# Kernel tuning notes

Hardware: AMD Instinct MI355X
Metric: run time of the kernel (lower is better)

## Reference

```python
import jax, jax.numpy as jnp
import numpy as np

N, B, E, H, D, L, NT = 30000, 16, 60000, 128, 64, 2, 5


def _build_graph():
    rng = np.random.default_rng(0)
    ng = N // B
    row = rng.integers(0, N, size=E)
    g = row // ng
    col = g * ng + rng.integers(0, ng, size=E)  # bonds stay within a graph
    order = np.argsort(g, kind='stable')        # sort bonds by graph id
    row, col = row[order], col[order]
    edge_index = np.stack([row, col]).astype(np.int32)
    # bond graph: bonds adjacent iff they share an atom (vectorized _build_bond_graph)
    atoms = np.concatenate([row, col])
    bonds = np.concatenate([np.arange(E), np.arange(E)])
    o2 = np.argsort(atoms, kind='stable')
    sb = bonds[o2]
    counts = np.bincount(atoms, minlength=N)
    offs = np.concatenate([[0], np.cumsum(counts)[:-1]])
    sq = counts * counts
    total = int(sq.sum())
    gid = np.repeat(np.arange(N), sq)
    poff = np.concatenate([[0], np.cumsum(sq)[:-1]])
    pos = np.arange(total) - np.repeat(poff, sq)
    c, o = counts[gid], offs[gid]
    ii, jj = pos // c, pos % c
    mask = ii != jj
    bond_edge_index = np.stack([sb[o + ii][mask], sb[o + jj][mask]]).astype(np.int32)
    batch = np.repeat(np.arange(B), ng).astype(np.int32)
    return edge_index, bond_edge_index, batch


def setup_inputs() -> dict:
    edge_index, bond_edge_index, batch = _build_graph()
    key = jax.random.key(0)
    ks = jax.random.split(key, 16)
    s = 0.05
    n = lambda k, shp: jax.random.normal(k, shp, jnp.float32) * s
    return {
        'atom_features': jax.random.normal(ks[0], (N, H), jnp.float32),
        'atom_pos': jax.random.normal(ks[1], (N, 3), jnp.float32),
        'atomic_numbers': jax.random.randint(ks[2], (N,), 1, 20, jnp.int32),
        'batch': jnp.asarray(batch),
        'edge_index': jnp.asarray(edge_index),
        'bond_edge_index': jnp.asarray(bond_edge_index),
        'iw1': n(ks[3], (2 * H, D)), 'ib1': jnp.zeros((D,), jnp.float32),
        'iw2': n(ks[4], (D, D)), 'ib2': jnp.zeros((D,), jnp.float32),
        'emb': n(ks[5], (L, NT, D)),
        'mw1': n(ks[6], (L, 3 * D, D)), 'mb1': jnp.zeros((L, D), jnp.float32),
        'mw2': n(ks[7], (L, D, D)), 'mb2': jnp.zeros((L, D), jnp.float32),
        'uw1': n(ks[8], (L, 2 * D, D)), 'ub1': jnp.zeros((L, D), jnp.float32),
        'uw2': n(ks[9], (L, D, D)), 'ub2': jnp.zeros((L, D), jnp.float32),
        'num_graphs': B,
    }


def reference(atom_features, atom_pos, iw1, ib1, iw2, ib2, emb, mw1, mb1, mw2, mb2,
              uw1, ub1, uw2, ub2, atomic_numbers, batch, edge_index, bond_edge_index,
              num_graphs):
    row, col = edge_index
    hi, hj = atom_features[row], atom_features[col]  # [E, H] gathers
    # bond_init MLP
    x = jax.nn.silu(jnp.concatenate([hi, hj], -1) @ iw1 + ib1) @ iw2 + ib2  # [E, D]
    # _classify_bonds: cosine-similarity thresholds (order matters, matches torch)
    ni = jnp.maximum(jnp.linalg.norm(hi, axis=-1), 1e-8)
    nj = jnp.maximum(jnp.linalg.norm(hj, axis=-1), 1e-8)
    sim = jnp.sum(hi * hj, -1) / (ni * nj)
    bt = jnp.where(sim > 0.8, 1, 0)
    bt = jnp.where(sim > 0.9, 2, bt)
    bt = jnp.where(sim < 0.3, 3, bt)
    src, dst = bond_edge_index  # x_j = x[src], x_i = x[dst]; aggregate at dst
    nb = x.shape[0]
    deg = jax.ops.segment_sum(jnp.ones(src.shape, jnp.float32), dst, num_segments=nb)
    denom = jnp.maximum(deg, 1.0)[:, None]  # PyG mean aggr: 0 for isolated nodes
    for l in range(mw1.shape[0]):
        te = emb[l][bt]  # [E, D] bond-type embedding
        msg_in = jnp.concatenate([x[dst], x[src], te[dst]], -1)  # [BE, 3D]
        msg = jax.nn.silu(msg_in @ mw1[l] + mb1[l]) @ mw2[l] + mb2[l]
        aggr = jax.ops.segment_sum(msg, dst, num_segments=nb) / denom
        upd_in = jnp.concatenate([aggr, x], -1)
        x = x + jax.nn.silu(upd_in @ uw1[l] + ub1[l]) @ uw2[l] + ub2[l]
    # pooling: edges are sorted by graph, so repeat_interleave == batch[row]
    bond_batch = batch[row]
    cnt = jax.ops.segment_sum(jnp.ones((nb,), jnp.float32), bond_batch, num_segments=num_graphs)
    gfeat = jax.ops.segment_sum(x, bond_batch, num_segments=num_graphs) / jnp.maximum(cnt, 1.0)[:, None]
    return x, gfeat
```

## Files before the change

kernel.cpp:

```cpp
#include <hip/hip_runtime.h>
#include <hip/hip_cooperative_groups.h>
#include <cstdint>
#include <cstddef>

namespace cg = cooperative_groups;

#define HDIM 128
#define DDIM 64
#define NTYPES 5
#define NGRAPHS 16
#define EPB 64
#define SCAP 1024
#define PREPB 132

typedef __attribute__((ext_vector_type(8))) short short8;
typedef __attribute__((ext_vector_type(4))) float f32x4;

static __device__ __forceinline__ short8 as_s8(uint4 u) {
    return __builtin_bit_cast(short8, u);
}

static __device__ __forceinline__ float silu_f(float v) {
    return v * __builtin_amdgcn_rcpf(1.0f + __expf(-v));
}

static __device__ __forceinline__ float4 ld4(const float* p) {
    return *reinterpret_cast<const float4*>(p);
}

static __device__ __forceinline__ void st4(float* p, float4 v) {
    *reinterpret_cast<float4*>(p) = v;
}

static __device__ __forceinline__ float4 add4(float4 a, float4 b) {
    return make_float4(a.x + b.x, a.y + b.y, a.z + b.z, a.w + b.w);
}

static __device__ __forceinline__ void silu_acc4(float4& s, float4 v) {
    s.x += silu_f(v.x);
    s.y += silu_f(v.y);
    s.z += silu_f(v.z);
    s.w += silu_f(v.w);
}

static __device__ __forceinline__ unsigned int bf16r(float f) {
    unsigned int u = __float_as_uint(f);
    return (u + 0x7FFFu + ((u >> 16) & 1u)) >> 16;
}
static __device__ __forceinline__ unsigned int cvtpk(float a, float b) {
    unsigned int r;
    asm("v_cvt_pk_bf16_f32 %0, %1, %2" : "=v"(r) : "v"(a), "v"(b));
    return r;
}
static __device__ __forceinline__ uint4 pack8(const float* f) {
    uint4 r;
    r.x = cvtpk(f[0], f[1]);
    r.y = cvtpk(f[2], f[3]);
    r.z = cvtpk(f[4], f[5]);
    r.w = cvtpk(f[6], f[7]);
    return r;
}
static __device__ __forceinline__ void unpack8(uint4 u, float4& a, float4& b) {
    a.x = __uint_as_float(u.x << 16);
    a.y = __uint_as_float(u.x & 0xFFFF0000u);
    a.z = __uint_as_float(u.y << 16);
    a.w = __uint_as_float(u.y & 0xFFFF0000u);
    b.x = __uint_as_float(u.z << 16);
    b.y = __uint_as_float(u.z & 0xFFFF0000u);
    b.z = __uint_as_float(u.w << 16);
    b.w = __uint_as_float(u.w & 0xFFFF0000u);
}

static __device__ __forceinline__ void hilo8(const float* f, uint4& h, uint4& lo) {
    h = pack8(f);
    float4 a, b;
    unpack8(h, a, b);
    lo.x = cvtpk(f[0] - a.x, f[1] - a.y);
    lo.y = cvtpk(f[2] - a.z, f[3] - a.w);
    lo.z = cvtpk(f[4] - b.x, f[5] - b.y);
    lo.w = cvtpk(f[6] - b.z, f[7] - b.w);
}

static __device__ __forceinline__ int xcd_logical_block() {
    int chunk = (int)(gridDim.x >> 3);
    return (int)(blockIdx.x & 7) * chunk + (int)(blockIdx.x >> 3);
}

__global__ void __launch_bounds__(256) bsum_k(const int* __restrict__ cnt,
                                              int* __restrict__ bsum, int E) {
    __shared__ int red[256];
    int t = threadIdx.x;
    int i = blockIdx.x * 256 + t;
    red[t] = (i < E) ? cnt[i] : 0;
    __syncthreads();
    #pragma unroll
    for (int off = 128; off > 0; off >>= 1) {
        if (t < off) red[t] += red[t + off];
        __syncthreads();
    }
    if (t == 0) bsum[blockIdx.x] = red[0];
}

__global__ void __launch_bounds__(1024) bscan_k(const int* __restrict__ bsum,
                                                int* __restrict__ bpre, int NB) {
    __shared__ int sh[1024];
    int t = threadIdx.x;
    int v0 = (t < NB) ? bsum[t] : 0;
    sh[t] = v0;
    __syncthreads();
    for (int off = 1; off < 1024; off <<= 1) {
        int v = (t >= off) ? sh[t - off] : 0;
        __syncthreads();
        sh[t] += v;
        __syncthreads();
    }
    if (t < NB) bpre[t] = sh[t] - v0;
}

__global__ void __launch_bounds__(256) offs_k(const int* __restrict__ cnt,
                                              const int* __restrict__ bpre,
                                              int* __restrict__ offs,
                                              int* __restrict__ cursor, int E) {
    __shared__ int sh[256];
    int t = threadIdx.x;
    int i = blockIdx.x * 256 + t;
    int v0 = (i < E) ? cnt[i] : 0;
    sh[t] = v0;
    __syncthreads();
    for (int off = 1; off < 256; off <<= 1) {
        int v = (t >= off) ? sh[t - off] : 0;
        __syncthreads();
        sh[t] += v;
        __syncthreads();
    }
    int ex = sh[t] - v0 + bpre[blockIdx.x];
    if (i < E) { offs[i] = ex; cursor[i] = ex; }
    if (i == E - 1) offs[E] = ex + v0;
}

__global__ void __launch_bounds__(256) scatter_k(const int* __restrict__ bsrc,
                                                 const int* __restrict__ bdst,
                                                 int* __restrict__ cursor,
                                                 int* __restrict__ srclist, int BE) {
    int i = blockIdx.x * 256 + threadIdx.x;
    if (i < BE) {
        int d = bdst[i];
        int p = __hip_atomic_fetch_add(&cursor[d], 1, __ATOMIC_RELAXED,
                                       __HIP_MEMORY_SCOPE_AGENT);
        srclist[p] = bsrc[i];
    }
}

static __device__ void dev_prep(int b, int l,
                                const float* __restrict__ emb,
                                const float* __restrict__ mw1,
                                const float* __restrict__ mb1,
                                const float* __restrict__ mw2,
                                const float* __restrict__ mb2,
                                const float* __restrict__ uw1,
                                const float* __restrict__ uw2,
                                const float* __restrict__ iw2,
                                const float* __restrict__ iw1,
                                float* __restrict__ tt,
                                float* __restrict__ b2u,
                                uint4* __restrict__ fw2u,
                                uint4* __restrict__ fu1b,
                                uint4* __restrict__ fu2,
                                uint4* __restrict__ fp,
                                uint4* __restrict__ fiw2,
                                uint4* __restrict__ fp0,
                                uint4* __restrict__ fiw1) {
    if (b < 10) {
        int ll = b / NTYPES, t = b % NTYPES;
        const float* embl = emb + (size_t)ll * NTYPES * DDIM + (size_t)t * DDIM;
        const float* w1 = mw1 + (size_t)ll * 192 * DDIM;
        float s = mb1[ll * DDIM + l];
        #pragma unroll 8
        for (int k = 0; k < DDIM; ++k)
            s = fmaf(embl[k], w1[(HDIM + k) * DDIM + l], s);
        tt[(size_t)b * DDIM + l] = s;
        return;
    }
    if (b < 12) {
        int ll = b - 10;
        const float* u1 = uw1 + (size_t)ll * 128 * DDIM;
        float s = 0.f;
        #pragma unroll 8
        for (int t = 0; t < DDIM; ++t)
            s = fmaf(mb2[ll * DDIM + t], u1[(size_t)t * DDIM + l], s);
        b2u[ll * DDIM + l] = s;
        return;
    }
    int pb = b - 12;
    int mat = pb >> 3, jt = (pb >> 1) & 3, ks = pb & 1;
    int k0 = ks * 32 + (l >> 4) * 8;
    int j = jt * 16 + (l & 15);
    float f[8];
    uint4* dst;
    if (mat <= 1) {
        const float* w2 = mw2 + (size_t)mat * DDIM * DDIM;
        const float* u1 = uw1 + (size_t)mat * 128 * DDIM;
        #pragma unroll
        for (int i = 0; i < 8; ++i) {
            float s = 0.f;
            #pragma unroll 8
            for (int t = 0; t < DDIM; ++t)
                s = fmaf(w2[(size_t)(k0 + i) * DDIM + t], u1[(size_t)t * DDIM + j], s);
            f[i] = s;
        }
        dst = fw2u + (size_t)mat * 1024;
    } else {
        const float* src;
        switch (mat) {
            case 2:  src = uw1 + 64 * 64;                    dst = fu1b;        break;
            case 3:  src = uw1 + 128 * 64 + 64 * 64;         dst = fu1b + 1024; break;
            case 4:  src = uw2;                              dst = fu2;         break;
            case 5:  src = uw2 + 4096;                       dst = fu2 + 1024;  break;
            case 6:  src = mw1 + (size_t)192 * 64;           dst = fp;          break;
            case 7:  src = mw1 + (size_t)192 * 64 + 64 * 64; dst = fp + 1024;   break;
            case 8:  src = iw2;                              dst = fiw2;        break;
            case 9:  src = mw1;                              dst = fp0;         break;
            case 10: src = mw1 + (size_t)64 * 64;            dst = fp0 + 1024;  break;
            case 11: src = iw1;                              dst = fiw1;        break;
            case 12: src = iw1 + (size_t)64 * 64;            dst = fiw1 + 1024; break;
            case 13: src = iw1 + (size_t)128 * 64;           dst = fiw1 + 2048; break;
            default: src = iw1 + (size_t)192 * 64;           dst = fiw1 + 3072; break;
        }
        #pragma unroll
        for (int i = 0; i < 8; ++i) f[i] = src[(size_t)(k0 + i) * DDIM + j];
    }
    uint4 h, lo;
    hilo8(f, h, lo);
    size_t di = ((size_t)(jt * 2 + ks) * 64 + l) * 2;
    dst[di] = h;
    dst[di + 1] = lo;
}

__global__ void __launch_bounds__(256) prepcount_k(
    const float* __restrict__ emb, const float* __restrict__ mw1,
    const float* __restrict__ mb1, const float* __restrict__ mw2,
    const float* __restrict__ mb2, const float* __restrict__ uw1,
    const float* __restrict__ uw2, const float* __restrict__ iw2,
    const float* __restrict__ iw1,
    float* __restrict__ tt, float* __restrict__ b2u,
    uint4* __restrict__ fw2u, uint4* __restrict__ fu1b, uint4* __restrict__ fu2,
    uint4* __restrict__ fp, uint4* __restrict__ fiw2, uint4* __restrict__ fp0,
    uint4* __restrict__ fiw1,
    const int* __restrict__ bdst, int* __restrict__ cnt, int BE) {
    int b = blockIdx.x;
    if (b < PREPB) {
        if (threadIdx.x < 64)
            dev_prep(b, threadIdx.x, emb, mw1, mb1, mw2, mb2, uw1, uw2, iw2, iw1,
                     tt, b2u, fw2u, fu1b, fu2, fp, fiw2, fp0, fiw1);
        return;
    }
    int i = (b - PREPB) * 256 + threadIdx.x;
    if (i < BE)
        __hip_atomic_fetch_add(&cnt[bdst[i]], 1, __ATOMIC_RELAXED, __HIP_MEMORY_SCOPE_AGENT);
}

static __device__ __forceinline__ int slotIdx(int row, int slot) {
    return row * 8 + (slot ^ (row & 7));
}
static __device__ __forceinline__ int slotIdx16(int row, int slot) {
    return row * 16 + (slot ^ (row & 7));
}

static __device__ __forceinline__ short8 ldFragA(const uint4* buf, int rowBase, int lane, int ks) {
    int row = rowBase + (lane & 15);
    int slot = ks * 4 + (lane >> 4);
    return as_s8(buf[slotIdx(row, slot)]);
}
static __device__ __forceinline__ short8 ldFragA16(const uint4* buf, int rowBase, int lane, int slot0) {
    int row = rowBase + (lane & 15);
    int slot = slot0 + (lane >> 4);
    return as_s8(buf[slotIdx16(row, slot)]);
}

static __device__ __forceinline__ void loadB(const uint4* __restrict__ frag, int jt, int lane,
                                             short8& h0, short8& h1, short8& l0, short8& l1) {
    const uint4* p0 = frag + ((size_t)(jt * 2 + 0) * 64 + lane) * 2;
    const uint4* p1 = frag + ((size_t)(jt * 2 + 1) * 64 + lane) * 2;
    h0 = as_s8(p0[0]); l0 = as_s8(p0[1]);
    h1 = as_s8(p1[0]); l1 = as_s8(p1[1]);
}

static __device__ __forceinline__ f32x4 gemm_tile(const uint4* Ahi, const uint4* Alo,
        int rowBase, int lane,
        short8 bh0, short8 bh1, short8 bl0, short8 bl1, f32x4 acc) {
    short8 ah0 = ldFragA(Ahi, rowBase, lane, 0);
    short8 ah1 = ldFragA(Ahi, rowBase, lane, 1);
    short8 al0 = ldFragA(Alo, rowBase, lane, 0);
    short8 al1 = ldFragA(Alo, rowBase, lane, 1);
    acc = __builtin_amdgcn_mfma_f32_16x16x32_bf16(ah0, bh0, acc, 0, 0, 0);
    acc = __builtin_amdgcn_mfma_f32_16x16x32_bf16(ah1, bh1, acc, 0, 0, 0);
    acc = __builtin_amdgcn_mfma_f32_16x16x32_bf16(al0, bh0, acc, 0, 0, 0);
    acc = __builtin_amdgcn_mfma_f32_16x16x32_bf16(al1, bh1, acc, 0, 0, 0);
    acc = __builtin_amdgcn_mfma_f32_16x16x32_bf16(ah0, bl0, acc, 0, 0, 0);
    acc = __builtin_amdgcn_mfma_f32_16x16x32_bf16(ah1, bl1, acc, 0, 0, 0);
    return acc;
}

static __device__ __forceinline__ f32x4 gemm_tile16(const uint4* Ahi, const uint4* Alo,
        int rowBase, int lane, int sb,
        short8 bh0, short8 bh1, short8 bl0, short8 bl1, f32x4 acc) {
    short8 ah0 = ldFragA16(Ahi, rowBase, lane, sb + 0);
    short8 ah1 = ldFragA16(Ahi, rowBase, lane, sb + 4);
    short8 al0 = ldFragA16(Alo, rowBase, lane, sb + 0);
    short8 al1 = ldFragA16(Alo, rowBase, lane, sb + 4);
    acc = __builtin_amdgcn_mfma_f32_16x16x32_bf16(ah0, bh0, acc, 0, 0, 0);
    acc = __builtin_amdgcn_mfma_f32_16x16x32_bf16(ah1, bh1, acc, 0, 0, 0);
    acc = __builtin_amdgcn_mfma_f32_16x16x32_bf16(al0, bh0, acc, 0, 0, 0);
    acc = __builtin_amdgcn_mfma_f32_16x16x32_bf16(al1, bh1, acc, 0, 0, 0);
    acc = __builtin_amdgcn_mfma_f32_16x16x32_bf16(ah0, bl0, acc, 0, 0, 0);
    acc = __builtin_amdgcn_mfma_f32_16x16x32_bf16(ah1, bl1, acc, 0, 0, 0);
    return acc;
}

static __device__ __forceinline__ void dev_atom_proj(
    int a0, int tid, int lane, int w,
    const float* __restrict__ AF, const uint4* __restrict__ fIw1,
    float* __restrict__ pa, float* __restrict__ qa, float* __restrict__ na, int N,
    uint4* sHi, uint4* sLo) {
    {
        int dl = tid >> 3, q = tid & 7;
        int a = a0 + dl;
        bool ok = a < N;
        const float* ar = AF + (size_t)(ok ? a : 0) * HDIM + q * 16;
        float4 v0 = ld4(ar + 0), v1 = ld4(ar + 4), v2 = ld4(ar + 8), v3 = ld4(ar + 12);
        float nrm = v0.x*v0.x + v0.y*v0.y + v0.z*v0.z + v0.w*v0.w
                  + v1.x*v1.x + v1.y*v1.y + v1.z*v1.z + v1.w*v1.w
                  + v2.x*v2.x + v2.y*v2.y + v2.z*v2.z + v2.w*v2.w
                  + v3.x*v3.x + v3.y*v3.y + v3.z*v3.z + v3.w*v3.w;
        nrm += __shfl_xor(nrm, 1, 64);
        nrm += __shfl_xor(nrm, 2, 64);
        nrm += __shfl_xor(nrm, 4, 64);
        if (q == 0 && ok) na[a] = sqrtf(nrm);
        float f0[8] = {v0.x, v0.y, v0.z, v0.w, v1.x, v1.y, v1.z, v1.w};
        float f1[8] = {v2.x, v2.y, v2.z, v2.w, v3.x, v3.y, v3.z, v3.w};
        if (!ok) {
            #pragma unroll
            for (int i = 0; i < 8; ++i) { f0[i] = 0.f; f1[i] = 0.f; }
        }
        uint4 h, l;
        hilo8(f0, h, l);
        int s0 = slotIdx16(dl, q * 2);
        sHi[s0] = h; sLo[s0] = l;
        hilo8(f1, h, l);
        int s1 = slotIdx16(dl, q * 2 + 1);
        sHi[s1] = h; sLo[s1] = l;
    }
    int jt = w & 3;
    const uint4* m0 = fIw1 + ((w < 4) ? 0 : 2048);
    short8 B0h0, B0h1, B0l0, B0l1, B1h0, B1h1, B1l0, B1l1;
    loadB(m0, jt, lane, B0h0, B0h1, B0l0, B0l1);
    loadB(m0 + 1024, jt, lane, B1h0, B1h1, B1l0, B1l1);
    __syncthreads();

    float* dst = (w < 4) ? pa : qa;
    int j = jt * 16 + (lane & 15);
    f32x4 z4 = {0.f, 0.f, 0.f, 0.f};
    #pragma unroll
    for (int rt = 0; rt < 4; ++rt) {
        f32x4 acc = gemm_tile16(sHi, sLo, rt * 16, lane, 0, B0h0, B0h1, B0l0, B0l1, z4);
        acc = gemm_tile16(sHi, sLo, rt * 16, lane, 8, B1h0, B1h1, B1l0, B1l1, acc);
        #pragma unroll
        for (int r = 0; r < 4; ++r) {
            int rowi = rt * 16 + (lane >> 4) * 4 + r;
            int a = a0 + rowi;
            if (a < N) dst[(size_t)a * DDIM + j] = acc[r];
        }
    }
}

__global__ void __launch_bounds__(512) atom_proj_k(
    const float* __restrict__ AF, const uint4* __restrict__ fIw1,
    float* __restrict__ pa, float* __restrict__ qa, float* __restrict__ na, int N) {
    __shared__ uint4 sHi[1024];
    __shared__ uint4 sLo[1024];
    int tid = threadIdx.x, lane = tid & 63;
    int w = __builtin_amdgcn_readfirstlane((int)(tid >> 6));
    int a0 = blockIdx.x * 64;
    if (a0 < N)
        dev_atom_proj(a0, tid, lane, w, AF, fIw1, pa, qa, na, N, sHi, sLo);
}

static __device__ __forceinline__ void dev_bond_init(
    int lb, int tid, int lane, int w,
    const float* __restrict__ AF, const int* __restrict__ row, const int* __restrict__ col,
    const float* __restrict__ pa, const float* __restrict__ qa, const float* __restrict__ na,
    const float* __restrict__ b1, const uint4* __restrict__ fW2, const float* __restrict__ b2,
    const uint4* __restrict__ fP0,
    float* __restrict__ x, int* __restrict__ bt,
    float* __restrict__ pd, uint4* __restrict__ ps, int E,
    uint4* sAhi, uint4* sAlo, uint4* sXhi, uint4* sXlo, bool storeX) {
    int e0 = lb * EPB;

    {
        int dl = tid >> 3, q = tid & 7;
        int d = e0 + dl;
        bool ok = d < E;
        int dd = ok ? d : 0;
        int r = row[dd], c = col[dd];
        int jq = q * 8;

        const float* hi = AF + (size_t)r * HDIM + q * 16;
        const float* hj = AF + (size_t)c * HDIM + q * 16;
        float dt = 0.f;
        #pragma unroll
        for (int k = 0; k < 16; k += 4) {
            float4 a4 = ld4(hi + k), b4 = ld4(hj + k);
            dt += a4.x * b4.x + a4.y * b4.y + a4.z * b4.z + a4.w * b4.w;
        }
        dt += __shfl_xor(dt, 1, 64);
        dt += __shfl_xor(dt, 2, 64);
        dt += __shfl_xor(dt, 4, 64);
        if (q == 0 && ok) {
            float nr = fmaxf(na[r], 1e-8f), nc = fmaxf(na[c], 1e-8f);
            float sim = dt / (nr * nc);
            int t = 0;
            if (sim > 0.8f) t = 1;
            if (sim > 0.9f) t = 2;
            if (sim < 0.3f) t = 3;
            bt[d] = t;
        }

        const float* pr = pa + (size_t)r * DDIM + jq;
        const float* qc = qa + (size_t)c * DDIM + jq;
        float4 p0 = ld4(pr + 0), p1 = ld4(pr + 4);
        float4 q0 = ld4(qc + 0), q1 = ld4(qc + 4);
        float hv[8];
        hv[0] = silu_f(p0.x + q0.x + b1[jq + 0]);
        hv[1] = silu_f(p0.y + q0.y + b1[jq + 1]);
        hv[2] = silu_f(p0.z + q0.z + b1[jq + 2]);
        hv[3] = silu_f(p0.w + q0.w + b1[jq + 3]);
        hv[4] = silu_f(p1.x + q1.x + b1[jq + 4]);
        hv[5] = silu_f(p1.y + q1.y + b1[jq + 5]);
        hv[6] = silu_f(p1.z + q1.z + b1[jq + 6]);
        hv[7] = silu_f(p1.w + q1.w + b1[jq + 7]);
        if (!ok) {
            #pragma unroll
            for (int i = 0; i < 8; ++i) hv[i] = 0.f;
        }
        uint4 h4, l4;
        hilo8(hv, h4, l4);
        int si = slotIdx(dl, q);
        sAhi[si] = h4; sAlo[si] = l4;
    }
    int jt = w & 3, mh = w >> 2;
    short8 W2h0, W2h1, W2l0, W2l1;
    loadB(fW2, jt, lane, W2h0, W2h1, W2l0, W2l1);
    __syncthreads();

    int rb0 = mh * 32, rb1 = mh * 32 + 16;
    f32x4 z4 = {0.f, 0.f, 0.f, 0.f};
    f32x4 acc0 = gemm_tile(sAhi, sAlo, rb0, lane, W2h0, W2h1, W2l0, W2l1, z4);
    f32x4 acc1 = gemm_tile(sAhi, sAlo, rb1, lane, W2h0, W2h1, W2l0, W2l1, z4);
    int j = jt * 16 + (lane & 15);
    float b2j = b2[j];
    unsigned short* hX = (unsigned short*)sXhi;
    unsigned short* lX = (unsigned short*)sXlo;
    #pragma unroll
    for (int r = 0; r < 4; ++r) {
        int rowi = rb0 + (lane >> 4) * 4 + r;
        int e = e0 + rowi;
        float xn = acc0[r] + b2j;
        if (storeX && e < E) x[(size_t)e * DDIM + j] = xn;
        unsigned int hb = bf16r(xn);
        float lov = xn - __uint_as_float(hb << 16);
        int ui = (rowi * 8 + ((j >> 3) ^ (rowi & 7))) * 8 + (j & 7);
        hX[ui] = (unsigned short)hb;
        lX[ui] = (unsigned short)bf16r(lov);
    }
    #pragma unroll
    for (int r = 0; r < 4; ++r) {
        int rowi = rb1 + (lane >> 4) * 4 + r;
        int e = e0 + rowi;
        float xn = acc1[r] + b2j;
        if (storeX && e < E) x[(size_t)e * DDIM + j] = xn;
        unsigned int hb = bf16r(xn);
        float lov = xn - __uint_as_float(hb << 16);
        int ui = (rowi * 8 + ((j >> 3) ^ (rowi & 7))) * 8 + (j & 7);
        hX[ui] = (unsigned short)hb;
        lX[ui] = (unsigned short)bf16r(lov);
    }
    __syncthreads();

    const uint4* fPw = (w < 4) ? fP0 : (fP0 + 1024);
    int jp = w & 3;
    short8 Ph0, Ph1, Pl0, Pl1;
    loadB(fPw, jp, lane, Ph0, Ph1, Pl0, Pl1);
    f32x4 q0 = gemm_tile(sXhi, sXlo, 0,  lane, Ph0, Ph1, Pl0, Pl1, z4);
    f32x4 q1 = gemm_tile(sXhi, sXlo, 16, lane, Ph0, Ph1, Pl0, Pl1, z4);
    f32x4 q2 = gemm_tile(sXhi, sXlo, 32, lane, Ph0, Ph1, Pl0, Pl1, z4);
    f32x4 q3 = gemm_tile(sXhi, sXlo, 48, lane, Ph0, Ph1, Pl0, Pl1, z4);
    unsigned short* hA = (unsigned short*)sAhi;
    if (w < 4) {
        int jd = jp * 16 + (lane & 15);
        #pragma unroll
        for (int mt = 0; mt < 4; ++mt) {
            f32x4 qq = (mt == 0) ? q0 : (mt == 1) ? q1 : (mt == 2) ? q2 : q3;
            #pragma unroll
            for (int r = 0; r < 4; ++r) {
                int rowi = mt * 16 + (lane >> 4) * 4 + r;
                int e = e0 + rowi;
                if (e < E) pd[(size_t)e * DDIM + jd] = qq[r];
            }
        }
    } else {
        int js = jp * 16 + (lane & 15);
        #pragma unroll
        for (int mt = 0; mt < 4; ++mt) {
            f32x4 qq = (mt == 0) ? q0 : (mt == 1) ? q1 : (mt == 2) ? q2 : q3;
            #pragma unroll
            for (int r = 0; r < 4; ++r) {
                int rowi = mt * 16 + (lane >> 4) * 4 + r;
                int ui = (rowi * 8 + ((js >> 3) ^ (rowi & 7))) * 8 + (js & 7);
                hA[ui] = (unsigned short)bf16r(qq[r]);
            }
        }
    }
    __syncthreads();
    {
        int dl = tid >> 3, q = tid & 7;
        int d = e0 + dl;
        if (d < E) ps[(size_t)d * 8 + q] = sAhi[slotIdx(dl, q)];
    }
}

__global__ void __launch_bounds__(512, 4) bond_init2_k(
    const float* __restrict__ AF, const int* __restrict__ row, const int* __restrict__ col,
    const float* __restrict__ pa, const float* __restrict__ qa, const float* __restrict__ na,
    const float* __restrict__ b1, const uint4* __restrict__ fW2, const float* __restrict__ b2,
    const uint4* __restrict__ fP0,
    float* __restrict__ x, int* __restrict__ bt,
    float* __restrict__ pd, uint4* __restrict__ ps, int E) {
    __shared__ uint4 sAhi[512];
    __shared__ uint4 sAlo[512];
    __shared__ uint4 sXhi[512];
    __shared__ uint4 sXlo[512];
    int nEB = (E + EPB - 1) / EPB;
    int lb = xcd_logical_block();
    if (lb >= nEB) return;
    int tid = threadIdx.x, lane = tid & 63;
    int w = __builtin_amdgcn_readfirstlane((int)(tid >> 6));
    dev_bond_init(lb, tid, lane, w, AF, row, col, pa, qa, na, b1, fW2, b2, fP0,
                  x, bt, pd, ps, E, sAhi, sAlo, sXhi, sXlo, true);
}

__global__ void __launch_bounds__(256) proj_k(const float* __restrict__ x,
                                              const float* __restrict__ w1 ,
                                              float* __restrict__ pd, uint4* __restrict__ ps,
                                              int E) {
    int lane = threadIdx.x & 63;
    int w = __builtin_amdgcn_readfirstlane((int)(threadIdx.x >> 6));
    int e = blockIdx.x * EPB + lane;
    bool ok = e < E;
    int eidx = ok ? e : 0;
    int j0 = w * 16;
    const float* xr = x + (size_t)eidx * DDIM;

    float apd[16], aps[16];
    #pragma unroll
    for (int jj = 0; jj < 16; ++jj) { apd[jj] = 0.f; aps[jj] = 0.f; }
    #pragma unroll 2
    for (int c = 0; c < 16; ++c) {
        float4 v = ld4(xr + c * 4);
        float xv[4] = {v.x, v.y, v.z, v.w};
        #pragma unroll
        for (int kk = 0; kk < 4; ++kk) {
            int k = c * 4 + kk;
            const float* wd = w1 + (size_t)k * DDIM + j0;
            const float* wsv = w1 + (size_t)(DDIM + k) * DDIM + j0;
            #pragma unroll
            for (int jj = 0; jj < 16; ++jj) {
                apd[jj] = fmaf(xv[kk], wd[jj], apd[jj]);
                aps[jj] = fmaf(xv[kk], wsv[jj], aps[jj]);
            }
        }
    }
    if (ok) {
        float* pr = pd + (size_t)e * DDIM + j0;
        st4(pr + 0,  make_float4(apd[0],  apd[1],  apd[2],  apd[3]));
        st4(pr + 4,  make_float4(apd[4],  apd[5],  apd[6],  apd[7]));
        st4(pr + 8,  make_float4(apd[8],  apd[9],  apd[10], apd[11]));
        st4(pr + 12, make_float4(apd[12], apd[13], apd[14], apd[15]));
        ps[(size_t)e * 8 + 2 * w + 0] = pack8(aps + 0);
        ps[(size_t)e * 8 + 2 * w + 1] = pack8(aps + 8);
    }
}

static __device__ __forceinline__ void dev_layer(
    int lb, int tid, int lane, int w,
    float* __restrict__ x, const float* __restrict__ pd, const uint4* __restrict__ ps,
    const float* __restrict__ tt_l, const int* __restrict__ bt,
    const int* __restrict__ offs, const int* __restrict__ srclist,
    const int* __restrict__ cnt,
    const uint4* __restrict__ fW2u, const float* __restrict__ b2u,
    const uint4* __restrict__ fU1b, const float* __restrict__ ub1,
    const uint4* __restrict__ fU2, const float* __restrict__ ub2,
    const uint4* __restrict__ fP, float* __restrict__ pdn, uint4* __restrict__ psn,
    int E, const int* __restrict__ erow, const int* __restrict__ gbatch,
    float* __restrict__ gfeat, int doPool,
    uint4* sAhi, uint4* sAlo, uint4* sXhi, uint4* sXlo,
    float* degLDS, int* gidLDS, int* sIdx, bool loadX, bool storeX3) {
    int e0 = lb * EPB;
    int pb0 = offs[e0];

    {
        int dl = tid >> 3, q = tid & 7;
        int d = e0 + dl;
        bool ok = d < E;
        int dd = ok ? d : 0;
        int jq = q * 8;
        float4 xv0 = make_float4(0, 0, 0, 0), xv1 = xv0;
        if (loadX) {
            const float* xr = x + (size_t)dd * DDIM + jq;
            xv0 = ld4(xr + 0); xv1 = ld4(xr + 4);
        }
        int dc = cnt[dd];
        int rAtom = (doPool && ok) ? erow[dd] : 0;
        const float* pr = pd + (size_t)dd * DDIM + jq;
        const float* tp = tt_l + (size_t)bt[dd] * DDIM + jq;
        float4 b0 = add4(ld4(pr + 0), ld4(tp + 0));
        float4 b1 = add4(ld4(pr + 4), ld4(tp + 4));
        int p0v = ok ? offs[d] : pb0, p1v = ok ? offs[d + 1] : pb0;

        int emax = min(e0 + EPB, E);
        int pT = offs[emax] - pb0;
        for (int i = tid; i < pT && i < SCAP; i += 512) sIdx[i] = srclist[pb0 + i];
        __syncthreads();

        float4 s0 = make_float4(0, 0, 0, 0), s1 = s0;
        if (p1v - pb0 <= SCAP) {
            int li = p0v - pb0, le = p1v - pb0;
            for (; li + 4 <= le; li += 4) {
                uint4 u0 = ps[(size_t)sIdx[li + 0] * 8 + q];
                uint4 u1 = ps[(size_t)sIdx[li + 1] * 8 + q];
                uint4 u2 = ps[(size_t)sIdx[li + 2] * 8 + q];
                uint4 u3 = ps[(size_t)sIdx[li + 3] * 8 + q];
                float4 a, b;
                unpack8(u0, a, b);
                silu_acc4(s0, add4(b0, a));
                silu_acc4(s1, add4(b1, b));
                unpack8(u1, a, b);
                silu_acc4(s0, add4(b0, a));
                silu_acc4(s1, add4(b1, b));
                unpack8(u2, a, b);
                silu_acc4(s0, add4(b0, a));
                silu_acc4(s1, add4(b1, b));
                unpack8(u3, a, b);
                silu_acc4(s0, add4(b0, a));
                silu_acc4(s1, add4(b1, b));
            }
            for (; li < le; ++li) {
                uint4 u0 = ps[(size_t)sIdx[li] * 8 + q];
                float4 a, b;
                unpack8(u0, a, b);
                silu_acc4(s0, add4(b0, a));
                silu_acc4(s1, add4(b1, b));
            }
        } else {
            int p = p0v;
            for (; p + 4 <= p1v; p += 4) {
                uint4 u0 = ps[(size_t)srclist[p + 0] * 8 + q];
                uint4 u1 = ps[(size_t)srclist[p + 1] * 8 + q];
                uint4 u2 = ps[(size_t)srclist[p + 2] * 8 + q];
                uint4 u3 = ps[(size_t)srclist[p + 3] * 8 + q];
                float4 a, b;
                unpack8(u0, a, b);
                silu_acc4(s0, add4(b0, a));
                silu_acc4(s1, add4(b1, b));
                unpack8(u1, a, b);
                silu_acc4(s0, add4(b0, a));
                silu_acc4(s1, add4(b1, b));
                unpack8(u2, a, b);
                silu_acc4(s0, add4(b0, a));
                silu_acc4(s1, add4(b1, b));
                unpack8(u3, a, b);
                silu_acc4(s0, add4(b0, a));
                silu_acc4(s1, add4(b1, b));
            }
            for (; p < p1v; ++p) {
                uint4 u0 = ps[(size_t)srclist[p] * 8 + q];
                float4 a, b;
                unpack8(u0, a, b);
                silu_acc4(s0, add4(b0, a));
                silu_acc4(s1, add4(b1, b));
            }
        }
        float inv = 1.0f / fmaxf((float)dc, 1.0f);
        float sv[8] = {s0.x * inv, s0.y * inv, s0.z * inv, s0.w * inv,
                       s1.x * inv, s1.y * inv, s1.z * inv, s1.w * inv};
        if (!ok) {
            #pragma unroll
            for (int i = 0; i < 8; ++i) sv[i] = 0.f;
        }
        uint4 h4, l4;
        int si = slotIdx(dl, q);
        hilo8(sv, h4, l4);
        sAhi[si] = h4; sAlo[si] = l4;
        if (loadX) {
            float xf[8] = {xv0.x, xv0.y, xv0.z, xv0.w, xv1.x, xv1.y, xv1.z, xv1.w};
            if (!ok) {
                #pragma unroll
                for (int i = 0; i < 8; ++i) xf[i] = 0.f;
            }
            hilo8(xf, h4, l4);
            sXhi[si] = h4; sXlo[si] = l4;
        }
        if (q == 0) {
            degLDS[dl] = (ok && dc > 0) ? 1.0f : 0.0f;
            gidLDS[dl] = (doPool && ok) ? gbatch[rAtom] : -1;
        }
    }
    int jt = w & 3, mh = w >> 2;
    short8 A2h0, A2h1, A2l0, A2l1;
    short8 U1h0, U1h1, U1l0, U1l1;
    loadB(fW2u, jt, lane, A2h0, A2h1, A2l0, A2l1);
    loadB(fU1b, jt, lane, U1h0, U1h1, U1l0, U1l1);
    __syncthreads();

    int rb0 = mh * 32, rb1 = mh * 32 + 16;
    f32x4 z4 = {0.f, 0.f, 0.f, 0.f};
    f32x4 acc0 = z4, acc1 = z4;
    acc0 = gemm_tile(sAhi, sAlo, rb0, lane, A2h0, A2h1, A2l0, A2l1, acc0);
    acc0 = gemm_tile(sXhi, sXlo, rb0, lane, U1h0, U1h1, U1l0, U1l1, acc0);
    acc1 = gemm_tile(sAhi, sAlo, rb1, lane, A2h0, A2h1, A2l0, A2l1, acc1);
    acc1 = gemm_tile(sXhi, sXlo, rb1, lane, U1h0, U1h1, U1l0, U1l1, acc1);
    __syncthreads();
    int j = jt * 16 + (lane & 15);
    float ub1j = ub1[j], b2uj = b2u[j];
    unsigned short* hA = (unsigned short*)sAhi;
    unsigned short* lA = (unsigned short*)sAlo;
    #pragma unroll
    for (int r = 0; r < 4; ++r) {
        int row = rb0 + (lane >> 4) * 4 + r;
        float hv = silu_f(acc0[r] + ub1j + degLDS[row] * b2uj);
        unsigned int hb = bf16r(hv);
        float lov = hv - __uint_as_float(hb << 16);
        int ui = (row * 8 + ((j >> 3) ^ (row & 7))) * 8 + (j & 7);
        hA[ui] = (unsigned short)hb;
        lA[ui] = (unsigned short)bf16r(lov);
    }
    #pragma unroll
    for (int r = 0; r < 4; ++r) {
        int row = rb1 + (lane >> 4) * 4 + r;
        float hv = silu_f(acc1[r] + ub1j + degLDS[row] * b2uj);
        unsigned int hb = bf16r(hv);
        float lov = hv - __uint_as_float(hb << 16);
        int ui = (row * 8 + ((j >> 3) ^ (row & 7))) * 8 + (j & 7);
        hA[ui] = (unsigned short)hb;
        lA[ui] = (unsigned short)bf16r(lov);
    }
    __syncthreads();

    short8 U2h0, U2h1, U2l0, U2l1;
    loadB(fU2, jt, lane, U2h0, U2h1, U2l0, U2l1);
    f32x4 o0 = gemm_tile(sAhi, sAlo, rb0, lane, U2h0, U2h1, U2l0, U2l1, z4);
    f32x4 o1 = gemm_tile(sAhi, sAlo, rb1, lane, U2h0, U2h1, U2l0, U2l1, z4);
    float ub2j = ub2[j];
    bool haveP = (fP != nullptr);
    unsigned short* hX = (unsigned short*)sXhi;
    unsigned short* lX = (unsigned short*)sXlo;
    float xnv0[4], xnv1[4];
    #pragma unroll
    for (int r = 0; r < 4; ++r) {
        int row = rb0 + (lane >> 4) * 4 + r;
        int e = e0 + row;
        int ui = (row * 8 + ((j >> 3) ^ (row & 7))) * 8 + (j & 7);
        float xvv = __uint_as_float((unsigned int)hX[ui] << 16)
                  + __uint_as_float((unsigned int)lX[ui] << 16);
        float xn = xvv + o0[r] + ub2j;
        xnv0[r] = xn;
        if (storeX3 && e < E) x[(size_t)e * DDIM + j] = xn;
        if (haveP) {
            unsigned int hb = bf16r(xn);
            float lov = xn - __uint_as_float(hb << 16);
            hX[ui] = (unsigned short)hb;
            lX[ui] = (unsigned short)bf16r(lov);
        }
    }
    #pragma unroll
    for (int r = 0; r < 4; ++r) {
        int row = rb1 + (lane >> 4) * 4 + r;
        int e = e0 + row;
        int ui = (row * 8 + ((j >> 3) ^ (row & 7))) * 8 + (j & 7);
        float xvv = __uint_as_float((unsigned int)hX[ui] << 16)
                  + __uint_as_float((unsigned int)lX[ui] << 16);
        float xn = xvv + o1[r] + ub2j;
        xnv1[r] = xn;
        if (storeX3 && e < E) x[(size_t)e * DDIM + j] = xn;
        if (haveP) {
            unsigned int hb = bf16r(xn);
            float lov = xn - __uint_as_float(hb << 16);
            hX[ui] = (unsigned short)hb;
            lX[ui] = (unsigned short)bf16r(lov);
        }
    }
    if (!haveP) {
        if (doPool) {
            __syncthreads();
            float* poolB = (float*)sAhi;
            if (tid < 256) poolB[tid] = 0.f;
            __syncthreads();
            int gid0 = gidLDS[0];
            bool uni = (gidLDS[EPB - 1] == gid0);
            if (uni) {
                float s = xnv0[0] + xnv0[1] + xnv0[2] + xnv0[3]
                        + xnv1[0] + xnv1[1] + xnv1[2] + xnv1[3];
                atomicAdd(&poolB[j], s);
            } else {
                #pragma unroll
                for (int r = 0; r < 4; ++r) {
                    int row = rb0 + (lane >> 4) * 4 + r;
                    int g = gidLDS[row];
                    if (g >= 0) {
                        int sl = g - gid0;
                        if (sl < 4) atomicAdd(&poolB[sl * DDIM + j], xnv0[r]);
                        else atomicAdd(&gfeat[(size_t)g * DDIM + j], xnv0[r]);
                    }
                }
                #pragma unroll
                for (int r = 0; r < 4; ++r) {
                    int row = rb1 + (lane >> 4) * 4 + r;
                    int g = gidLDS[row];
                    if (g >= 0) {
                        int sl = g - gid0;
                        if (sl < 4) atomicAdd(&poolB[sl * DDIM + j], xnv1[r]);
                        else atomicAdd(&gfeat[(size_t)g * DDIM + j], xnv1[r]);
                    }
                }
            }
            __syncthreads();
            if (tid < 256) {
                int sl = tid >> 6;
                int g = gid0 + sl;
                float v = poolB[tid];
                if (v != 0.f && g < NGRAPHS)
                    atomicAdd(&gfeat[(size_t)g * DDIM + (tid & 63)], v);
            }
        }
        return;
    }
    __syncthreads();

    const uint4* fPw = (w < 4) ? fP : (fP + 1024);
    int jp = w & 3;
    short8 Ph0, Ph1, Pl0, Pl1;
    loadB(fPw, jp, lane, Ph0, Ph1, Pl0, Pl1);
    f32x4 q0 = gemm_tile(sXhi, sXlo, 0,  lane, Ph0, Ph1, Pl0, Pl1, z4);
    f32x4 q1 = gemm_tile(sXhi, sXlo, 16, lane, Ph0, Ph1, Pl0, Pl1, z4);
    f32x4 q2 = gemm_tile(sXhi, sXlo, 32, lane, Ph0, Ph1, Pl0, Pl1, z4);
    f32x4 q3 = gemm_tile(sXhi, sXlo, 48, lane, Ph0, Ph1, Pl0, Pl1, z4);
    if (w < 4) {
        int jd = jp * 16 + (lane & 15);
        #pragma unroll
        for (int mt = 0; mt < 4; ++mt) {
            f32x4 qq = (mt == 0) ? q0 : (mt == 1) ? q1 : (mt == 2) ? q2 : q3;
            #pragma unroll
            for (int r = 0; r < 4; ++r) {
                int row = mt * 16 + (lane >> 4) * 4 + r;
                int e = e0 + row;
                if (e < E) pdn[(size_t)e * DDIM + jd] = qq[r];
            }
        }
    } else {
        int js = jp * 16 + (lane & 15);
        #pragma unroll
        for (int mt = 0; mt < 4; ++mt) {
            f32x4 qq = (mt == 0) ? q0 : (mt == 1) ? q1 : (mt == 2) ? q2 : q3;
            #pragma unroll
            for (int r = 0; r < 4; ++r) {
                int row = mt * 16 + (lane >> 4) * 4 + r;
                int ui = (row * 8 + ((js >> 3) ^ (row & 7))) * 8 + (js & 7);
                hA[ui] = (unsigned short)bf16r(qq[r]);
            }
        }
    }
    __syncthreads();
    {
        int dl = tid >> 3, q = tid & 7;
        int d = e0 + dl;
        if (d < E) psn[(size_t)d * 8 + q] = sAhi[slotIdx(dl, q)];
    }
}

__global__ void __launch_bounds__(512, 4) layer_k(
    float* __restrict__ x, const float* __restrict__ pd, const uint4* __restrict__ ps,
    const float* __restrict__ tt_l, const int* __restrict__ bt,
    const int* __restrict__ offs, const int* __restrict__ srclist,
    const int* __restrict__ cnt,
    const uint4* __restrict__ fW2u, const float* __restrict__ b2u,
    const uint4* __restrict__ fU1b, const float* __restrict__ ub1,
    const uint4* __restrict__ fU2, const float* __restrict__ ub2,
    const uint4* __restrict__ fP,
    float* __restrict__ pdn, uint4* __restrict__ psn, int E,
    const int* __restrict__ erow, const int* __restrict__ gbatch,
    float* __restrict__ gfeat, int doPool) {
    __shared__ uint4 sAhi[512];
    __shared__ uint4 sAlo[512];
    __shared__ uint4 sXhi[512];
    __shared__ uint4 sXlo[512];
    __shared__ float degLDS[64];
    __shared__ int   gidLDS[64];
    __shared__ int   sIdx[SCAP];
    int nEB = (E + EPB - 1) / EPB;
    int lb = xcd_logical_block();
    if (lb >= nEB) return;
    int tid = threadIdx.x, lane = tid & 63;
    int w = __builtin_amdgcn_readfirstlane((int)(tid >> 6));
    dev_layer(lb, tid, lane, w, x, pd, ps, tt_l, bt, offs, srclist, cnt,
              fW2u, b2u, fU1b, ub1, fU2, ub2, fP, pdn, psn, E,
              erow, gbatch, gfeat, doPool,
              sAhi, sAlo, sXhi, sXlo, degLDS, gidLDS, sIdx, true, true);
}

static __device__ __forceinline__ int lower_bound_bb(const int* __restrict__ row,
                                                     const int* __restrict__ batch,
                                                     int E, int g) {
    int lo = 0, hi = E;
    while (lo < hi) {
        int m = (lo + hi) >> 1;
        if (batch[row[m]] < g) lo = m + 1; else hi = m;
    }
    return lo;
}

__global__ void __launch_bounds__(64) pool_final_k(
    const int* __restrict__ row, const int* __restrict__ batch,
    float* __restrict__ gfeat, int E) {
    int g = blockIdx.x, j = threadIdx.x;
    int s = lower_bound_bb(row, batch, E, g);
    int t = lower_bound_bb(row, batch, E, g + 1);
    float cnt = fmaxf((float)(t - s), 1.0f);
    gfeat[g * DDIM + j] /= cnt;
}

__global__ void __launch_bounds__(512, 8) fused_k(
    float* x, const int* row, const int* col,
    const float* AF, const uint4* fIw1, float* pa, float* qa, float* na, int N,
    const float* ib1, const uint4* fIw2, const float* ib2, const uint4* fP0,
    int* bt, float* pd, uint4* ps,
    const float* tt, const int* offs, const int* srclist, const int* cnt,
    const uint4* fW2u, const float* b2u, const uint4* fU1b, const float* ub1,
    const uint4* fU2, const float* ub2, const uint4* fP,
    float* pd2, uint4* ps2,
    const int* gbatch, float* gfeat, int E) {
    __shared__ uint4 U1[1024];
    __shared__ uint4 U2[1024];
    __shared__ float degLDS[64];
    __shared__ int   gidLDS[64];
    __shared__ int   sIdx[SCAP];
    cg::grid_group grid = cg::this_grid();
    int tid = threadIdx.x, lane = tid & 63;
    int w = __builtin_amdgcn_readfirstlane((int)(tid >> 6));
    uint4* sAhi = U1;
    uint4* sAlo = U1 + 512;
    uint4* sXhi = U2;
    uint4* sXlo = U2 + 512;

    if ((int)blockIdx.x * 64 < N)
        dev_atom_proj((int)blockIdx.x * 64, tid, lane, w, AF, fIw1, pa, qa, na, N, U1, U2);
    if (blockIdx.x == gridDim.x - 1)
        for (int i = tid; i < NGRAPHS * DDIM; i += 512) gfeat[i] = 0.f;
    __threadfence();
    grid.sync();

    int nEB = (E + EPB - 1) / EPB;
    int lb = xcd_logical_block();

    if (lb < nEB)
        dev_bond_init(lb, tid, lane, w, AF, row, col, pa, qa, na, ib1, fIw2, ib2, fP0,
                      x, bt, pd, ps, E, sAhi, sAlo, sXhi, sXlo, false);
    __threadfence();
    grid.sync();

    if (lb < nEB)
        dev_layer(lb, tid, lane, w, x, pd, ps, tt, bt, offs, srclist, cnt,
                  fW2u, b2u, fU1b, ub1, fU2, ub2, fP, pd2, ps2, E,
                  row, gbatch, gfeat, 0,
                  sAhi, sAlo, sXhi, sXlo, degLDS, gidLDS, sIdx, false, false);
    __threadfence();
    grid.sync();

    if (lb < nEB)
        dev_layer(lb, tid, lane, w, x, pd2, ps2, tt + NTYPES * DDIM, bt, offs, srclist, cnt,
                  fW2u + 1024, b2u + DDIM, fU1b + 1024, ub1 + DDIM,
                  fU2 + 1024, ub2 + DDIM, nullptr, nullptr, nullptr, E,
                  row, gbatch, gfeat, 1,
                  sAhi, sAlo, sXhi, sXlo, degLDS, gidLDS, sIdx, false, true);
    __threadfence();
    grid.sync();

    if ((int)blockIdx.x < NGRAPHS && tid < 64) {
        int g = blockIdx.x, j = tid;
        int s = lower_bound_bb(row, gbatch, E, g);
        int t = lower_bound_bb(row, gbatch, E, g + 1);
        float c = fmaxf((float)(t - s), 1.0f);
        gfeat[g * DDIM + j] /= c;
    }
}

extern "C" void kernel_launch(void* const* d_in, const int* in_sizes, int n_in,
                              void* d_out, int out_size, void* d_ws, size_t ws_size,
                              hipStream_t stream) {
    (void)n_in; (void)out_size;
    const float* AF    = (const float*)d_in[0];
    const int*   batch = (const int*)d_in[3];
    const int*   edge_index      = (const int*)d_in[4];
    const int*   bond_edge_index = (const int*)d_in[5];
    const float* iw1 = (const float*)d_in[6];
    const float* ib1 = (const float*)d_in[7];
    const float* iw2 = (const float*)d_in[8];
    const float* ib2 = (const float*)d_in[9];
    const float* emb = (const float*)d_in[10];
    const float* mw1 = (const float*)d_in[11];
    const float* mb1 = (const float*)d_in[12];
    const float* mw2 = (const float*)d_in[13];
    const float* mb2 = (const float*)d_in[14];
    const float* uw1 = (const float*)d_in[15];
    const float* ub1 = (const float*)d_in[16];
    const float* uw2 = (const float*)d_in[17];
    const float* ub2 = (const float*)d_in[18];

    const int N  = in_sizes[0] / HDIM;
    const int E  = in_sizes[4] / 2;
    const int BE = in_sizes[5] / 2;
    const int NB = (E + 255) / 256;
    const int EB = (E + EPB - 1) / EPB;
    const int APB = (N + 63) / 64;
    const int EBS = ((EB + 7) / 8) * 8;
    const int CNTB = (BE + 255) / 256;

    float* xout  = (float*)d_out;
    float* gfeat = xout + (size_t)E * DDIM;

    char* w = (char*)d_ws;
    float* tt       = (float*)w;  w += sizeof(float) * 2 * NTYPES * DDIM;
    float* b2u      = (float*)w;  w += sizeof(float) * 2 * DDIM;
    w = (char*)(((uintptr_t)w + 15) & ~(uintptr_t)15);
    uint4* fW2u     = (uint4*)w;  w += 2048 * sizeof(uint4);
    uint4* fU1b     = (uint4*)w;  w += 2048 * sizeof(uint4);
    uint4* fU2      = (uint4*)w;  w += 2048 * sizeof(uint4);
    uint4* fP       = (uint4*)w;  w += 2048 * sizeof(uint4);
    uint4* fIw2     = (uint4*)w;  w += 1024 * sizeof(uint4);
    uint4* fP0      = (uint4*)w;  w += 2048 * sizeof(uint4);
    uint4* fIw1     = (uint4*)w;  w += 4096 * sizeof(uint4);
    int*   cnt      = (int*)w;    w += sizeof(int) * E;
    int*   offs     = (int*)w;    w += sizeof(int) * (E + 1);
    int*   cursor   = (int*)w;    w += sizeof(int) * E;
    int*   bt       = (int*)w;    w += sizeof(int) * E;
    int*   srclist  = (int*)w;    w += sizeof(int) * BE;
    int*   bsum     = (int*)w;    w += sizeof(int) * 1024;
    int*   bpre     = (int*)w;    w += sizeof(int) * 1024;
    w = (char*)(((uintptr_t)w + 15) & ~(uintptr_t)15);
    float* pd       = (float*)w;  w += sizeof(float) * (size_t)E * DDIM;
    uint4* ps       = (uint4*)w;  w += sizeof(unsigned short) * (size_t)E * DDIM;
    float* pa       = (float*)w;  w += sizeof(float) * (size_t)N * DDIM;
    float* qa       = (float*)w;  w += sizeof(float) * (size_t)N * DDIM;
    float* na       = (float*)w;  w += sizeof(float) * (size_t)N;
    w = (char*)(((uintptr_t)w + 15) & ~(uintptr_t)15);
    float* pd2      = (float*)w;  w += sizeof(float) * (size_t)E * DDIM;
    uint4* ps2      = (uint4*)w;  w += sizeof(unsigned short) * (size_t)E * DDIM;
    bool fuse_proj = ((size_t)(w - (char*)d_ws) <= ws_size);

    const int* row  = edge_index;
    const int* col  = edge_index + E;
    const int* bsrc = bond_edge_index;
    const int* bdst = bond_edge_index + BE;

    hipMemsetAsync(cnt, 0, (size_t)E * sizeof(int), stream);
    prepcount_k<<<PREPB + CNTB, 256, 0, stream>>>(
        emb, mw1, mb1, mw2, mb2, uw1, uw2, iw2, iw1,
        tt, b2u, fW2u, fU1b, fU2, fP, fIw2, fP0, fIw1, bdst, cnt, BE);
    bsum_k<<<NB, 256, 0, stream>>>(cnt, bsum, E);
    bscan_k<<<1, 1024, 0, stream>>>(bsum, bpre, NB);
    offs_k<<<NB, 256, 0, stream>>>(cnt, bpre, offs, cursor, E);
    scatter_k<<<(BE + 255) / 256, 256, 0, stream>>>(bsrc, bdst, cursor, srclist, BE);

    static int s_coopBlocks = -1;
    if (s_coopBlocks < 0) {
        int dev = 0;
        hipGetDevice(&dev);
        int coopAttr = 0;
        hipDeviceGetAttribute(&coopAttr, hipDeviceAttributeCooperativeLaunch, dev);
        int nCU = 0;
        hipDeviceGetAttribute(&nCU, hipDeviceAttributeMultiprocessorCount, dev);
        int mb = 0;
        hipError_t oe = hipOccupancyMaxActiveBlocksPerMultiprocessor(&mb, fused_k, 512, 0);
        s_coopBlocks = (coopAttr && oe == hipSuccess && nCU > 0) ? mb * nCU : 0;
    }

    bool coopDone = false;
    if (fuse_proj && s_coopBlocks >= EBS) {
        int Nv = N, Ev = E;
        void* kargs[] = {
            (void*)&xout, (void*)&row, (void*)&col,
            (void*)&AF, (void*)&fIw1, (void*)&pa, (void*)&qa, (void*)&na, (void*)&Nv,
            (void*)&ib1, (void*)&fIw2, (void*)&ib2, (void*)&fP0,
            (void*)&bt, (void*)&pd, (void*)&ps,
            (void*)&tt, (void*)&offs, (void*)&srclist, (void*)&cnt,
            (void*)&fW2u, (void*)&b2u, (void*)&fU1b, (void*)&ub1,
            (void*)&fU2, (void*)&ub2, (void*)&fP,
            (void*)&pd2, (void*)&ps2,
            (void*)&batch, (void*)&gfeat, (void*)&Ev };
        hipError_t le = hipLaunchCooperativeKernel((const void*)fused_k, dim3(EBS),
                                                   dim3(512), kargs, 0, stream);
        coopDone = (le == hipSuccess);
    }

    if (!coopDone) {
        atom_proj_k<<<APB, 512, 0, stream>>>(AF, fIw1, pa, qa, na, N);
        bond_init2_k<<<EBS, 512, 0, stream>>>(AF, row, col, pa, qa, na, ib1, fIw2, ib2,
                                              fP0, xout, bt, pd, ps, E);
        hipMemsetAsync(gfeat, 0, NGRAPHS * DDIM * sizeof(float), stream);
        if (fuse_proj) {
            layer_k<<<EBS, 512, 0, stream>>>(
                xout, pd, ps, tt, bt, offs, srclist, cnt,
                fW2u, b2u, fU1b, ub1, fU2, ub2,
                fP, pd2, ps2, E, row, batch, gfeat, 0);
            layer_k<<<EBS, 512, 0, stream>>>(
                xout, pd2, ps2, tt + NTYPES * DDIM, bt, offs, srclist, cnt,
                fW2u + 1024, b2u + DDIM, fU1b + 1024, ub1 + DDIM,
                fU2 + 1024, ub2 + DDIM,
                nullptr, nullptr, nullptr, E, row, batch, gfeat, 1);
        } else {
            for (int l = 0; l < 2; ++l) {
                if (l > 0)
                    proj_k<<<EB, 256, 0, stream>>>(xout, mw1 + (size_t)l * 192 * 64, pd, ps, E);
                layer_k<<<EBS, 512, 0, stream>>>(
                    xout, pd, ps, tt + (size_t)l * NTYPES * DDIM, bt, offs, srclist, cnt,
                    fW2u + (size_t)l * 1024, b2u + (size_t)l * DDIM,
                    fU1b + (size_t)l * 1024, ub1 + (size_t)l * DDIM,
                    fU2 + (size_t)l * 1024, ub2 + (size_t)l * DDIM,
                    nullptr, nullptr, nullptr, E, row, batch, gfeat, l == 1 ? 1 : 0);
            }
        }
        pool_final_k<<<NGRAPHS, 64, 0, stream>>>(row, batch, gfeat, E);
    }
}
```

Baseline: 280.0 us.

## Fold CSR build (count, scan, scatter) into cooperative fused kernel phases

Moves the bond-graph CSR construction (degree counting, block sums, prefix scan, offsets and scatter of source indices) from five separate kernel launches plus a memset into extra phases of the cooperative fused kernel, separated by grid syncs. The count zeroing is folded into the weight-prep kernel, and counting overlaps with the atom projection phase. This removes several launch and drain gaps but adds three more grid-wide barriers and a single-block scan phase. Legacy launches are kept for the non-cooperative fallback.

```diff
diff --git a/kernel.cpp b/kernel.cpp
--- a/kernel.cpp
+++ b/kernel.cpp
@@ -84,6 +84,13 @@
 static __device__ __forceinline__ int xcd_logical_block() {
     int chunk = (int)(gridDim.x >> 3);
     return (int)(blockIdx.x & 7) * chunk + (int)(blockIdx.x >> 3);
+}
+
+__global__ void __launch_bounds__(256) count_k(const int* __restrict__ bdst,
+                                               int* __restrict__ cnt, int BE) {
+    int i = blockIdx.x * 256 + threadIdx.x;
+    if (i < BE)
+        __hip_atomic_fetch_add(&cnt[bdst[i]], 1, __ATOMIC_RELAXED, __HIP_MEMORY_SCOPE_AGENT);
 }
 
 __global__ void __launch_bounds__(256) bsum_k(const int* __restrict__ cnt,
@@ -236,7 +243,7 @@
     dst[di + 1] = lo;
 }
 
-__global__ void __launch_bounds__(256) prepcount_k(
+__global__ void __launch_bounds__(256) prep_k(
     const float* __restrict__ emb, const float* __restrict__ mw1,
     const float* __restrict__ mb1, const float* __restrict__ mw2,
     const float* __restrict__ mb2, const float* __restrict__ uw1,
@@ -245,18 +252,12 @@
     float* __restrict__ tt, float* __restrict__ b2u,
     uint4* __restrict__ fw2u, uint4* __restrict__ fu1b, uint4* __restrict__ fu2,
     uint4* __restrict__ fp, uint4* __restrict__ fiw2, uint4* __restrict__ fp0,
-    uint4* __restrict__ fiw1,
-    const int* __restrict__ bdst, int* __restrict__ cnt, int BE) {
-    int b = blockIdx.x;
-    if (b < PREPB) {
-        if (threadIdx.x < 64)
-            dev_prep(b, threadIdx.x, emb, mw1, mb1, mw2, mb2, uw1, uw2, iw2, iw1,
-                     tt, b2u, fw2u, fu1b, fu2, fp, fiw2, fp0, fiw1);
-        return;
-    }
-    int i = (b - PREPB) * 256 + threadIdx.x;
-    if (i < BE)
-        __hip_atomic_fetch_add(&cnt[bdst[i]], 1, __ATOMIC_RELAXED, __HIP_MEMORY_SCOPE_AGENT);
+    uint4* __restrict__ fiw1, int* __restrict__ cnt, int E) {
+    for (int i = blockIdx.x * 256 + threadIdx.x; i < E; i += gridDim.x * 256)
+        cnt[i] = 0;
+    if (threadIdx.x < 64)
+        dev_prep(blockIdx.x, threadIdx.x, emb, mw1, mb1, mw2, mb2, uw1, uw2, iw2, iw1,
+                 tt, b2u, fw2u, fu1b, fu2, fp, fiw2, fp0, fiw1);
 }
 
 static __device__ __forceinline__ int slotIdx(int row, int slot) {
@@ -942,11 +943,13 @@
     const float* AF, const uint4* fIw1, float* pa, float* qa, float* na, int N,
     const float* ib1, const uint4* fIw2, const float* ib2, const uint4* fP0,
     int* bt, float* pd, uint4* ps,
-    const float* tt, const int* offs, const int* srclist, const int* cnt,
+    const float* tt, int* offs, int* srclist, int* cnt,
     const uint4* fW2u, const float* b2u, const uint4* fU1b, const float* ub1,
     const uint4* fU2, const float* ub2, const uint4* fP,
     float* pd2, uint4* ps2,
-    const int* gbatch, float* gfeat, int E) {
+    const int* gbatch, float* gfeat, int E,
+    const int* bsrc, const int* bdst, int BE,
+    int* bsum, int* bpre, int* cursor) {
     __shared__ uint4 U1[1024];
     __shared__ uint4 U2[1024];
     __shared__ float degLDS[64];
@@ -959,20 +962,88 @@
     uint4* sAlo = U1 + 512;
     uint4* sXhi = U2;
     uint4* sXlo = U2 + 512;
+    int nEB = (E + EPB - 1) / EPB;
+    int lb = xcd_logical_block();
 
     if ((int)blockIdx.x * 64 < N)
         dev_atom_proj((int)blockIdx.x * 64, tid, lane, w, AF, fIw1, pa, qa, na, N, U1, U2);
+    for (int i = (int)blockIdx.x * 512 + tid; i < BE; i += (int)gridDim.x * 512)
+        __hip_atomic_fetch_add(&cnt[bdst[i]], 1, __ATOMIC_RELAXED, __HIP_MEMORY_SCOPE_AGENT);
     if (blockIdx.x == gridDim.x - 1)
         for (int i = tid; i < NGRAPHS * DDIM; i += 512) gfeat[i] = 0.f;
     __threadfence();
     grid.sync();
 
-    int nEB = (E + EPB - 1) / EPB;
-    int lb = xcd_logical_block();
-
-    if (lb < nEB)
+    if (lb < nEB) {
         dev_bond_init(lb, tid, lane, w, AF, row, col, pa, qa, na, ib1, fIw2, ib2, fP0,
                       x, bt, pd, ps, E, sAhi, sAlo, sXhi, sXlo, false);
+        if (tid < 64) {
+            int e = lb * EPB + tid;
+            int v = (e < E) ? cnt[e] : 0;
+            v += __shfl_xor(v, 1, 64);
+            v += __shfl_xor(v, 2, 64);
+            v += __shfl_xor(v, 4, 64);
+            v += __shfl_xor(v, 8, 64);
+            v += __shfl_xor(v, 16, 64);
+            v += __shfl_xor(v, 32, 64);
+            if (tid == 0) bsum[lb] = v;
+        }
+    }
+    __threadfence();
+    grid.sync();
+
+    if (blockIdx.x == 0) {
+        for (int i = tid; i < SCAP; i += 512) sIdx[i] = (i < nEB) ? bsum[i] : 0;
+        __syncthreads();
+        for (int off = 1; off < SCAP; off <<= 1) {
+            int i2 = tid + 512;
+            int v0 = (tid >= off) ? sIdx[tid - off] : 0;
+            int v1 = sIdx[i2 - off];
+            __syncthreads();
+            sIdx[tid] += v0;
+            sIdx[i2] += v1;
+            __syncthreads();
+        }
+        for (int i = tid; i < nEB; i += 512) bpre[i] = sIdx[i] - bsum[i];
+    }
+    __threadfence();
+    grid.sync();
+
+    if (lb < nEB) {
+        int e0 = lb * EPB;
+        int myc = 0;
+        if (tid < 64) {
+            int e = e0 + tid;
+            myc = (e < E) ? cnt[e] : 0;
+            gidLDS[tid] = myc;
+        }
+        __syncthreads();
+        for (int off = 1; off < 64; off <<= 1) {
+            int v = 0;
+            if (tid < 64 && tid >= off) v = gidLDS[tid - off];
+            __syncthreads();
+            if (tid < 64) gidLDS[tid] += v;
+            __syncthreads();
+        }
+        if (tid < 64) {
+            int e = e0 + tid;
+            if (e < E) {
+                int ex = gidLDS[tid] - myc + bpre[lb];
+                offs[e] = ex;
+                cursor[e] = ex;
+                if (e == E - 1) offs[E] = ex + myc;
+            }
+        }
+    }
+    __threadfence();
+    grid.sync();
+
+    for (int i = (int)blockIdx.x * 512 + tid; i < BE; i += (int)gridDim.x * 512) {
+        int d = bdst[i];
+        int p = __hip_atomic_fetch_add(&cursor[d], 1, __ATOMIC_RELAXED,
+                                       __HIP_MEMORY_SCOPE_AGENT);
+        srclist[p] = bsrc[i];
+    }
     __threadfence();
     grid.sync();
 
@@ -1029,6 +1100,7 @@
     const int BE = in_sizes[5] / 2;
     const int NB = (E + 255) / 256;
     const int EB = (E + EPB - 1) / EPB;
+    const int nEB = EB;
     const int APB = (N + 63) / 64;
     const int EBS = ((EB + 7) / 8) * 8;
     const int CNTB = (BE + 255) / 256;
@@ -1070,14 +1142,9 @@
     const int* bsrc = bond_edge_index;
     const int* bdst = bond_edge_index + BE;
 
-    hipMemsetAsync(cnt, 0, (size_t)E * sizeof(int), stream);
-    prepcount_k<<<PREPB + CNTB, 256, 0, stream>>>(
-        emb, mw1, mb1, mw2, mb2, uw1, uw2, iw2, iw1,
-        tt, b2u, fW2u, fU1b, fU2, fP, fIw2, fP0, fIw1, bdst, cnt, BE);
-    bsum_k<<<NB, 256, 0, stream>>>(cnt, bsum, E);
-    bscan_k<<<1, 1024, 0, stream>>>(bsum, bpre, NB);
-    offs_k<<<NB, 256, 0, stream>>>(cnt, bpre, offs, cursor, E);
-    scatter_k<<<(BE + 255) / 256, 256, 0, stream>>>(bsrc, bdst, cursor, srclist, BE);
+    prep_k<<<PREPB, 256, 0, stream>>>(emb, mw1, mb1, mw2, mb2, uw1, uw2, iw2, iw1,
+                                      tt, b2u, fW2u, fU1b, fU2, fP, fIw2, fP0, fIw1,
+                                      cnt, E);
 
     static int s_coopBlocks = -1;
     if (s_coopBlocks < 0) {
@@ -1093,8 +1160,8 @@
     }
 
     bool coopDone = false;
-    if (fuse_proj && s_coopBlocks >= EBS) {
-        int Nv = N, Ev = E;
+    if (fuse_proj && s_coopBlocks >= EBS && nEB <= SCAP) {
+        int Nv = N, Ev = E, BEv = BE;
         void* kargs[] = {
             (void*)&xout, (void*)&row, (void*)&col,
             (void*)&AF, (void*)&fIw1, (void*)&pa, (void*)&qa, (void*)&na, (void*)&Nv,
@@ -1104,13 +1171,20 @@
             (void*)&fW2u, (void*)&b2u, (void*)&fU1b, (void*)&ub1,
             (void*)&fU2, (void*)&ub2, (void*)&fP,
             (void*)&pd2, (void*)&ps2,
-            (void*)&batch, (void*)&gfeat, (void*)&Ev };
+            (void*)&batch, (void*)&gfeat, (void*)&Ev,
+            (void*)&bsrc, (void*)&bdst, (void*)&BEv,
+            (void*)&bsum, (void*)&bpre, (void*)&cursor };
         hipError_t le = hipLaunchCooperativeKernel((const void*)fused_k, dim3(EBS),
                                                    dim3(512), kargs, 0, stream);
         coopDone = (le == hipSuccess);
     }
 
     if (!coopDone) {
+        count_k<<<CNTB, 256, 0, stream>>>(bdst, cnt, BE);
+        bsum_k<<<NB, 256, 0, stream>>>(cnt, bsum, E);
+        bscan_k<<<1, 1024, 0, stream>>>(bsum, bpre, NB);
+        offs_k<<<NB, 256, 0, stream>>>(cnt, bpre, offs, cursor, E);
+        scatter_k<<<(BE + 255) / 256, 256, 0, stream>>>(bsrc, bdst, cursor, srclist, BE);
         atom_proj_k<<<APB, 512, 0, stream>>>(AF, fIw1, pa, qa, na, N);
         bond_init2_k<<<EBS, 512, 0, stream>>>(AF, row, col, pa, qa, na, ib1, fIw2, ib2,
                                               fP0, xout, bt, pd, ps, E);
```

New measurement: 280.6 us. No clear change (+0.2%).
